# Kernel optimization log

Measured on AMD Instinct MI355X. Metric: run time of the kernel, lower is better.

The kernel has to match this reference:

```python
import jax, jax.numpy as jnp
import numpy as np

HEADS = 8
NEG_SLOPE = 0.2  # PyG GATConv default negative_slope


def segment_softmax(logits, seg, num_segments):
    # logits: [E, H], seg: [E] destination ids
    m = jax.ops.segment_max(logits, seg, num_segments=num_segments)
    m = jnp.where(jnp.isfinite(m), m, 0.0)
    e = jnp.exp(logits - jax.lax.stop_gradient(m)[seg])
    s = jax.ops.segment_sum(e, seg, num_segments=num_segments)
    return e / (s[seg] + 1e-16)


def setup_inputs() -> dict:
    key = jax.random.key(0)
    k1, k2, k3, k4, k5, k6 = jax.random.split(key, 6)
    N, F_IN, H, C, E = 50000, 116, HEADS, 32, 800000
    x = jax.random.normal(k1, (N, F_IN), dtype=jnp.float32)
    edge_index = jax.random.randint(k2, (2, E), 0, N, dtype=jnp.int64)
    # Params (glorot-ish scale)
    W = jax.random.normal(k3, (F_IN, H * C), dtype=jnp.float32) * (1.0 / np.sqrt(F_IN))
    att_src = jax.random.normal(k4, (1, H, C), dtype=jnp.float32) * (1.0 / np.sqrt(C))
    att_dst = jax.random.normal(k5, (1, H, C), dtype=jnp.float32) * (1.0 / np.sqrt(C))
    bias = jnp.zeros((C,), dtype=jnp.float32)
    return {"x": x, "edge_index": edge_index, "W": W, "att_src": att_src, "att_dst": att_dst, "bias": bias}


def reference(x, edge_index, W, att_src, att_dst, bias):
    N = x.shape[0]
    H = HEADS
    C = W.shape[1] // H
    # Shared linear transform: [N, H, C]
    xt = (x @ W).reshape(N, H, C)
    alpha_src = jnp.sum(xt * att_src, axis=-1)  # [N, H]
    alpha_dst = jnp.sum(xt * att_dst, axis=-1)  # [N, H]
    # add_self_loops=True (PyG GATConv default)
    loops = jnp.arange(N, dtype=edge_index.dtype)
    src = jnp.concatenate([edge_index[0], loops])
    dst = jnp.concatenate([edge_index[1], loops])
    # Edge-wise attention logits + segment softmax over destination
    alpha = jax.nn.leaky_relu(alpha_src[src] + alpha_dst[dst], negative_slope=NEG_SLOPE)  # [E', H]
    alpha = segment_softmax(alpha, dst, N)
    # Weighted message aggregation
    msg = xt[src] * alpha[:, :, None]  # [E', H, C]
    out = jax.ops.segment_sum(msg, dst, num_segments=N)  # [N, H, C]
    # concat=False -> mean over heads, then bias
    out = out.mean(axis=1) + bias  # [N, C]
    return jax.nn.relu(out)
```

## Files before the change

kernel.cpp:

```cpp
#include <hip/hip_runtime.h>
#include <hip/hip_bf16.h>


#define F_IN 116
#define HC 256
#define NHEAD 8
#define CDIM 32
#define KP 128
#define ROWS_PB 48
#define DSLOT 64
#define ECHUNK 4096

typedef unsigned int uint32;
typedef short short8 __attribute__((ext_vector_type(8)));
typedef float f32x4 __attribute__((ext_vector_type(4)));

__device__ __forceinline__ unsigned short f2bf(float f) {
    uint32 u = __float_as_uint(f);
    u = (u + 0x7FFF + ((u >> 16) & 1)) >> 16;
    return (unsigned short)u;
}

__global__ void init_k(const float* __restrict__ W,
                       const float* __restrict__ att_s,
                       const float* __restrict__ att_d,
                       unsigned short* __restrict__ WbT,
                       unsigned short* __restrict__ WaT) {
    int idx = blockIdx.x * 256 + threadIdx.x;
    if (idx < 32768) {
        int n = idx >> 7, k = idx & 127;
        WbT[idx] = (k < F_IN) ? f2bf(W[k * HC + n]) : (unsigned short)0;
    } else {
        int aid = idx - 32768;
        int col = aid >> 7, k = aid & 127;
        int tile = col >> 4;
        int cc = col & 15;
        int h = cc & 7, part = cc >> 3;
        const float* att = tile ? att_d : att_s;
        float s = 0.f;
        if (k < F_IN) {
            for (int c = 0; c < CDIM; ++c)
                s = fmaf(W[k * HC + h * CDIM + c], att[h * CDIM + c], s);
        }
        unsigned short hi = f2bf(s);
        unsigned short v = hi;
        if (part) {
            float rem = s - __uint_as_float((uint32)hi << 16);
            v = f2bf(rem);
        }
        WaT[col * KP + k] = v;
    }
}

__global__ __launch_bounds__(256) void scatter_k(const int* __restrict__ src,
                                                 const int* __restrict__ dst,
                                                 int* __restrict__ cnt,
                                                 unsigned short* __restrict__ csr,
                                                 int N, int E) {
    const int t = threadIdx.x;
    const int slice = blockIdx.x & 7;
    const int chunk = blockIdx.x >> 3;
    const int SLICE = (N + 7) >> 3;
    const int lo = slice * SLICE;
    const int hi = (lo + SLICE < N) ? lo + SLICE : N;
    const int ebase = chunk * ECHUNK + t * 4;
#pragma unroll
    for (int it = 0; it < ECHUNK / 1024; ++it) {
        int e = ebase + it * 1024;
        if (e < E) {
            int4 d4 = *(const int4*)&dst[e];
            int4 s4 = *(const int4*)&src[e];
            if (d4.x >= lo && d4.x < hi) {
                int r = atomicAdd(&cnt[d4.x], 1);
                if (r < DSLOT) csr[(d4.x << 6) + r] = (unsigned short)s4.x;
            }
            if (d4.y >= lo && d4.y < hi) {
                int r = atomicAdd(&cnt[d4.y], 1);
                if (r < DSLOT) csr[(d4.y << 6) + r] = (unsigned short)s4.y;
            }
            if (d4.z >= lo && d4.z < hi) {
                int r = atomicAdd(&cnt[d4.z], 1);
                if (r < DSLOT) csr[(d4.z << 6) + r] = (unsigned short)s4.z;
            }
            if (d4.w >= lo && d4.w < hi) {
                int r = atomicAdd(&cnt[d4.w], 1);
                if (r < DSLOT) csr[(d4.w << 6) + r] = (unsigned short)s4.w;
            }
        }
    }
}

__global__ __launch_bounds__(256) void gemm_k(const float* __restrict__ x,
                                              const unsigned short* __restrict__ WbT,
                                              const unsigned short* __restrict__ WaT,
                                              unsigned short* __restrict__ xth,
                                              float* __restrict__ asrc,
                                              float* __restrict__ adst,
                                              int N) {
    const int t = threadIdx.x;
    __shared__ unsigned short xbs[16 * ROWS_PB * 8];
    const int row0 = blockIdx.x * ROWS_PB;
    for (int u = t; u < 16 * ROWS_PB; u += 256) {
        const int g = u / ROWS_PB, r = u - g * ROWS_PB;
        const int gr = row0 + r;
        f32x4 v0 = {0.f, 0.f, 0.f, 0.f}, v1 = {0.f, 0.f, 0.f, 0.f};
        if (gr < N) {
            const f32x4* xp = (const f32x4*)(x + (size_t)gr * F_IN + g * 8);
            if (g < 14) { v0 = xp[0]; v1 = xp[1]; }
            else if (g == 14) { v0 = xp[0]; }
        }
        short8 pk;
        pk[0] = (short)f2bf(v0.x); pk[1] = (short)f2bf(v0.y);
        pk[2] = (short)f2bf(v0.z); pk[3] = (short)f2bf(v0.w);
        pk[4] = (short)f2bf(v1.x); pk[5] = (short)f2bf(v1.y);
        pk[6] = (short)f2bf(v1.z); pk[7] = (short)f2bf(v1.w);
        *(short8*)&xbs[u * 8] = pk;
    }
    __syncthreads();

    const int w = t >> 6, l = t & 63;
    const int q = l >> 4, m = l & 15;
    const int ncol0 = w * 64;

    short8 bfr[4][4];
#pragma unroll
    for (int nt = 0; nt < 4; ++nt)
#pragma unroll
        for (int ks = 0; ks < 4; ++ks)
            bfr[nt][ks] = *(const short8*)&WbT[(size_t)(ncol0 + nt * 16 + m) * KP + ks * 32 + q * 8];

    short8 wa[4];
    if (w < 2) {
#pragma unroll
        for (int ks = 0; ks < 4; ++ks)
            wa[ks] = *(const short8*)&WaT[(size_t)(w * 16 + m) * KP + ks * 32 + q * 8];
    }

    f32x4 acc[3][4];
#pragma unroll
    for (int rt = 0; rt < 3; ++rt)
#pragma unroll
        for (int nt = 0; nt < 4; ++nt) acc[rt][nt] = f32x4{0.f, 0.f, 0.f, 0.f};
    f32x4 acc_a[3];
#pragma unroll
    for (int rt = 0; rt < 3; ++rt) acc_a[rt] = f32x4{0.f, 0.f, 0.f, 0.f};

#pragma unroll
    for (int ks = 0; ks < 4; ++ks) {
        short8 a[3];
#pragma unroll
        for (int rt = 0; rt < 3; ++rt)
            a[rt] = *(const short8*)&xbs[((ks * 4 + q) * ROWS_PB + rt * 16 + m) * 8];
#pragma unroll
        for (int nt = 0; nt < 4; ++nt)
#pragma unroll
            for (int rt = 0; rt < 3; ++rt)
                acc[rt][nt] = __builtin_amdgcn_mfma_f32_16x16x32_bf16(bfr[nt][ks], a[rt], acc[rt][nt], 0, 0, 0);
        if (w < 2) {
#pragma unroll
            for (int rt = 0; rt < 3; ++rt)
                acc_a[rt] = __builtin_amdgcn_mfma_f32_16x16x32_bf16(wa[ks], a[rt], acc_a[rt], 0, 0, 0);
        }
    }

#pragma unroll
    for (int rt = 0; rt < 3; ++rt) {
        const int row = row0 + rt * 16 + m;
        if (row < N) {
#pragma unroll
            for (int nt = 0; nt < 4; ++nt) {
                uint2 pk;
                pk.x = (uint32)f2bf(acc[rt][nt][0]) | ((uint32)f2bf(acc[rt][nt][1]) << 16);
                pk.y = (uint32)f2bf(acc[rt][nt][2]) | ((uint32)f2bf(acc[rt][nt][3]) << 16);
                *(uint2*)&xth[(size_t)row * HC + ncol0 + nt * 16 + q * 4] = pk;
            }
        }
    }

    if (w < 2) {
        float* ap = (w == 0) ? asrc : adst;
#pragma unroll
        for (int rt = 0; rt < 3; ++rt) {
            f32x4 s;
#pragma unroll
            for (int r = 0; r < 4; ++r) {
                float v = acc_a[rt][r];
                s[r] = v + __shfl_xor(v, 32, 64);
            }
            const int row = row0 + rt * 16 + m;
            if (q < 2 && row < N)
                *(f32x4*)&ap[row * NHEAD + q * 4] = s;
        }
    }
}

__global__ __launch_bounds__(256) void aggregate_k(const unsigned short* __restrict__ xth,
                                                   const float* __restrict__ asrc,
                                                   const float* __restrict__ adst,
                                                   const int* __restrict__ cnt,
                                                   const unsigned short* __restrict__ csr,
                                                   const float* __restrict__ bias,
                                                   float* __restrict__ out, int N) {
    const int t = threadIdx.x;
    const int lg = t & 31;
    const int base = t & 32;
    const int n = blockIdx.x * 8 + (t >> 5);
    if (n >= N) return;

    const int h_f = lg >> 2;
    const int h_w = lg & 7;
    const int e_w = lg >> 3;

    const int beg = n << 6;
    int d = cnt[n];
    if (d > DSLOT) d = DSLOT;

    const float adst_hw = adst[n * NHEAD + h_w];

    float zs = asrc[n * NHEAD + h_f] + adst[n * NHEAD + h_f];
    zs = (zs > 0.f) ? zs : 0.2f * zs;
    const float wself = __expf(zs);

    uint4 sv = ((const uint4*)(xth + (size_t)n * HC))[lg];
    float a0 = wself * __uint_as_float(sv.x << 16);
    float a1 = wself * __uint_as_float(sv.x & 0xFFFF0000u);
    float a2 = wself * __uint_as_float(sv.y << 16);
    float a3 = wself * __uint_as_float(sv.y & 0xFFFF0000u);
    float a4 = wself * __uint_as_float(sv.z << 16);
    float a5 = wself * __uint_as_float(sv.z & 0xFFFF0000u);
    float a6 = wself * __uint_as_float(sv.w << 16);
    float a7 = wself * __uint_as_float(sv.w & 0xFFFF0000u);
    float wsum = wself;

    const int nfull = d >> 2;
    const int rem = d & 3;
    int pos = beg;
    for (int cch = 0; cch < nfull; ++cch, pos += 4) {
        int s_w = (int)csr[pos + e_w];
        float z = asrc[s_w * NHEAD + h_w] + adst_hw;
        z = (z > 0.f) ? z : 0.2f * z;
        float w_reg = __expf(z);
#pragma unroll
        for (int e = 0; e < 4; ++e) {
            int s = __shfl(s_w, base + (e << 3), 64);
            float w = __shfl(w_reg, base + (e << 3) + h_f, 64);
            uint4 v = ((const uint4*)(xth + (size_t)s * HC))[lg];
            a0 = fmaf(w, __uint_as_float(v.x << 16), a0);
            a1 = fmaf(w, __uint_as_float(v.x & 0xFFFF0000u), a1);
            a2 = fmaf(w, __uint_as_float(v.y << 16), a2);
            a3 = fmaf(w, __uint_as_float(v.y & 0xFFFF0000u), a3);
            a4 = fmaf(w, __uint_as_float(v.z << 16), a4);
            a5 = fmaf(w, __uint_as_float(v.z & 0xFFFF0000u), a5);
            a6 = fmaf(w, __uint_as_float(v.w << 16), a6);
            a7 = fmaf(w, __uint_as_float(v.w & 0xFFFF0000u), a7);
            wsum += w;
        }
    }
    if (rem) {
        int s_w = (e_w < rem) ? (int)csr[pos + e_w] : n;
        float z = asrc[s_w * NHEAD + h_w] + adst_hw;
        z = (z > 0.f) ? z : 0.2f * z;
        float w_reg = __expf(z);
        for (int e = 0; e < rem; ++e) {
            int s = __shfl(s_w, base + (e << 3), 64);
            float w = __shfl(w_reg, base + (e << 3) + h_f, 64);
            uint4 v = ((const uint4*)(xth + (size_t)s * HC))[lg];
            a0 = fmaf(w, __uint_as_float(v.x << 16), a0);
            a1 = fmaf(w, __uint_as_float(v.x & 0xFFFF0000u), a1);
            a2 = fmaf(w, __uint_as_float(v.y << 16), a2);
            a3 = fmaf(w, __uint_as_float(v.y & 0xFFFF0000u), a3);
            a4 = fmaf(w, __uint_as_float(v.z << 16), a4);
            a5 = fmaf(w, __uint_as_float(v.z & 0xFFFF0000u), a5);
            a6 = fmaf(w, __uint_as_float(v.w << 16), a6);
            a7 = fmaf(w, __uint_as_float(v.w & 0xFFFF0000u), a7);
            wsum += w;
        }
    }

    const float inv = 1.f / (wsum + 1e-16f);
    a0 *= inv; a1 *= inv; a2 *= inv; a3 *= inv;
    a4 *= inv; a5 *= inv; a6 *= inv; a7 *= inv;

#pragma unroll
    for (int o = 4; o <= 16; o <<= 1) {
        a0 += __shfl_xor(a0, o, 64);
        a1 += __shfl_xor(a1, o, 64);
        a2 += __shfl_xor(a2, o, 64);
        a3 += __shfl_xor(a3, o, 64);
        a4 += __shfl_xor(a4, o, 64);
        a5 += __shfl_xor(a5, o, 64);
        a6 += __shfl_xor(a6, o, 64);
        a7 += __shfl_xor(a7, o, 64);
    }

    if (lg < 4) {
        const float* bp = bias + 8 * lg;
        float4 r0, r1;
        r0.x = fmaxf(a0 * 0.125f + bp[0], 0.f);
        r0.y = fmaxf(a1 * 0.125f + bp[1], 0.f);
        r0.z = fmaxf(a2 * 0.125f + bp[2], 0.f);
        r0.w = fmaxf(a3 * 0.125f + bp[3], 0.f);
        r1.x = fmaxf(a4 * 0.125f + bp[4], 0.f);
        r1.y = fmaxf(a5 * 0.125f + bp[5], 0.f);
        r1.z = fmaxf(a6 * 0.125f + bp[6], 0.f);
        r1.w = fmaxf(a7 * 0.125f + bp[7], 0.f);
        *(float4*)&out[(size_t)n * CDIM + 8 * lg] = r0;
        *(float4*)&out[(size_t)n * CDIM + 8 * lg + 4] = r1;
    }
}

extern "C" void kernel_launch(void* const* d_in, const int* in_sizes, int n_in,
                              void* d_out, int out_size, void* d_ws, size_t ws_size,
                              hipStream_t stream) {
    const float* x     = (const float*)d_in[0];
    const int*   ei    = (const int*)d_in[1];
    const float* W     = (const float*)d_in[2];
    const float* att_s = (const float*)d_in[3];
    const float* att_d = (const float*)d_in[4];
    const float* bias  = (const float*)d_in[5];
    float* out = (float*)d_out;

    const int N = in_sizes[0] / F_IN;
    const int E = in_sizes[1] / 2;

    unsigned short* xth = (unsigned short*)d_ws;
    unsigned short* WbT = xth + (size_t)N * HC;
    float* asrc = (float*)(WbT + 256 * KP);
    float* adst = asrc + (size_t)N * NHEAD;
    int*   cnt  = (int*)(adst + (size_t)N * NHEAD);
    unsigned short* csr = (unsigned short*)(cnt + N);
    unsigned short* WaT = csr + (size_t)N * DSLOT;

    const int Ggemm = (N + ROWS_PB - 1) / ROWS_PB;
    const int nchunk = (E + ECHUNK - 1) / ECHUNK;
    const int Gscat = nchunk * 8;

    (void)hipMemsetAsync(cnt, 0, (size_t)N * sizeof(int), stream);
    init_k<<<144, 256, 0, stream>>>(W, att_s, att_d, WbT, WaT);
    scatter_k<<<Gscat, 256, 0, stream>>>(ei, ei + E, cnt, csr, N, E);
    gemm_k<<<Ggemm, 256, 0, stream>>>(x, WbT, WaT, xth, asrc, adst, N);
    aggregate_k<<<(N + 7) / 8, 256, 0, stream>>>(xth, asrc, adst, cnt, csr, bias, out, N);
}
```

Before: 209.9 us.

## Fuse edge scatter and GEMM into one interleaved kernel, fold memset into init

Merges the CSR-building scatter kernel and the feature-transform GEMM kernel into a single launch. Block groups are interleaved in a 3:2 scatter-to-GEMM pattern so the atomic-heavy scatter and the compute-heavy GEMM run at the same time on the GPU. Zeroing of the per-node counters moves from a separate memset into the init kernel. This saves two launches and lets two independent stages overlap, at the cost of a larger fused kernel whose register and LDS footprint applies to scatter blocks too. Any cycles where one side is exhausted leave early-exiting blocks.

```diff
diff --git a/kernel.cpp b/kernel.cpp
--- a/kernel.cpp
+++ b/kernel.cpp
@@ -25,8 +25,10 @@
                        const float* __restrict__ att_s,
                        const float* __restrict__ att_d,
                        unsigned short* __restrict__ WbT,
-                       unsigned short* __restrict__ WaT) {
+                       unsigned short* __restrict__ WaT,
+                       int* __restrict__ cnt, int N) {
     int idx = blockIdx.x * 256 + threadIdx.x;
+    for (int i = idx; i < N; i += 144 * 256) cnt[i] = 0;
     if (idx < 32768) {
         int n = idx >> 7, k = idx & 127;
         WbT[idx] = (k < F_IN) ? f2bf(W[k * HC + n]) : (unsigned short)0;
@@ -52,62 +54,71 @@
     }
 }
 
-__global__ __launch_bounds__(256) void scatter_k(const int* __restrict__ src,
-                                                 const int* __restrict__ dst,
-                                                 int* __restrict__ cnt,
-                                                 unsigned short* __restrict__ csr,
-                                                 int N, int E) {
-    const int t = threadIdx.x;
-    const int slice = blockIdx.x & 7;
-    const int chunk = blockIdx.x >> 3;
-    const int SLICE = (N + 7) >> 3;
-    const int lo = slice * SLICE;
-    const int hi = (lo + SLICE < N) ? lo + SLICE : N;
-    const int ebase = chunk * ECHUNK + t * 4;
-#pragma unroll
-    for (int it = 0; it < ECHUNK / 1024; ++it) {
-        int e = ebase + it * 1024;
-        if (e < E) {
-            int4 d4 = *(const int4*)&dst[e];
-            int4 s4 = *(const int4*)&src[e];
-            if (d4.x >= lo && d4.x < hi) {
-                int r = atomicAdd(&cnt[d4.x], 1);
-                if (r < DSLOT) csr[(d4.x << 6) + r] = (unsigned short)s4.x;
-            }
-            if (d4.y >= lo && d4.y < hi) {
-                int r = atomicAdd(&cnt[d4.y], 1);
-                if (r < DSLOT) csr[(d4.y << 6) + r] = (unsigned short)s4.y;
-            }
-            if (d4.z >= lo && d4.z < hi) {
-                int r = atomicAdd(&cnt[d4.z], 1);
-                if (r < DSLOT) csr[(d4.z << 6) + r] = (unsigned short)s4.z;
-            }
-            if (d4.w >= lo && d4.w < hi) {
-                int r = atomicAdd(&cnt[d4.w], 1);
-                if (r < DSLOT) csr[(d4.w << 6) + r] = (unsigned short)s4.w;
-            }
-        }
-    }
-}
-
-__global__ __launch_bounds__(256) void gemm_k(const float* __restrict__ x,
+__global__ __launch_bounds__(256) void fuse_k(const float* __restrict__ x,
                                               const unsigned short* __restrict__ WbT,
                                               const unsigned short* __restrict__ WaT,
                                               unsigned short* __restrict__ xth,
                                               float* __restrict__ asrc,
                                               float* __restrict__ adst,
-                                              int N) {
+                                              int N, int nScatGrp, int Ggemm,
+                                              const int* __restrict__ src,
+                                              const int* __restrict__ dst,
+                                              int* __restrict__ cnt,
+                                              unsigned short* __restrict__ csr, int E) {
     const int t = threadIdx.x;
+    const int g = blockIdx.x >> 3, r = blockIdx.x & 7;
+    const int c = g / 5, p = g - c * 5;
+
+    if (p < 3) {
+        const int sg = c * 3 + p;
+        if (sg >= nScatGrp) return;
+        const int sbid = sg * 8 + r;
+        const int slice = sbid & 7;
+        const int chunk = sbid >> 3;
+        const int SLICE = (N + 7) >> 3;
+        const int lo = slice * SLICE;
+        const int hi = (lo + SLICE < N) ? lo + SLICE : N;
+        const int ebase = chunk * ECHUNK + t * 4;
+#pragma unroll
+        for (int it = 0; it < ECHUNK / 1024; ++it) {
+            int e = ebase + it * 1024;
+            if (e < E) {
+                int4 d4 = *(const int4*)&dst[e];
+                int4 s4 = *(const int4*)&src[e];
+                if (d4.x >= lo && d4.x < hi) {
+                    int rr = atomicAdd(&cnt[d4.x], 1);
+                    if (rr < DSLOT) csr[(d4.x << 6) + rr] = (unsigned short)s4.x;
+                }
+                if (d4.y >= lo && d4.y < hi) {
+                    int rr = atomicAdd(&cnt[d4.y], 1);
+                    if (rr < DSLOT) csr[(d4.y << 6) + rr] = (unsigned short)s4.y;
+                }
+                if (d4.z >= lo && d4.z < hi) {
+                    int rr = atomicAdd(&cnt[d4.z], 1);
+                    if (rr < DSLOT) csr[(d4.z << 6) + rr] = (unsigned short)s4.z;
+                }
+                if (d4.w >= lo && d4.w < hi) {
+                    int rr = atomicAdd(&cnt[d4.w], 1);
+                    if (rr < DSLOT) csr[(d4.w << 6) + rr] = (unsigned short)s4.w;
+                }
+            }
+        }
+        return;
+    }
+
+    const int gbid = (c * 2 + (p - 3)) * 8 + r;
+    if (gbid >= Ggemm) return;
+
     __shared__ unsigned short xbs[16 * ROWS_PB * 8];
-    const int row0 = blockIdx.x * ROWS_PB;
+    const int row0 = gbid * ROWS_PB;
     for (int u = t; u < 16 * ROWS_PB; u += 256) {
-        const int g = u / ROWS_PB, r = u - g * ROWS_PB;
-        const int gr = row0 + r;
+        const int gg = u / ROWS_PB, rr = u - gg * ROWS_PB;
+        const int gr = row0 + rr;
         f32x4 v0 = {0.f, 0.f, 0.f, 0.f}, v1 = {0.f, 0.f, 0.f, 0.f};
         if (gr < N) {
-            const f32x4* xp = (const f32x4*)(x + (size_t)gr * F_IN + g * 8);
-            if (g < 14) { v0 = xp[0]; v1 = xp[1]; }
-            else if (g == 14) { v0 = xp[0]; }
+            const f32x4* xp = (const f32x4*)(x + (size_t)gr * F_IN + gg * 8);
+            if (gg < 14) { v0 = xp[0]; v1 = xp[1]; }
+            else if (gg == 14) { v0 = xp[0]; }
         }
         short8 pk;
         pk[0] = (short)f2bf(v0.x); pk[1] = (short)f2bf(v0.y);
@@ -183,9 +194,9 @@
         for (int rt = 0; rt < 3; ++rt) {
             f32x4 s;
 #pragma unroll
-            for (int r = 0; r < 4; ++r) {
-                float v = acc_a[rt][r];
-                s[r] = v + __shfl_xor(v, 32, 64);
+            for (int rr = 0; rr < 4; ++rr) {
+                float v = acc_a[rt][rr];
+                s[rr] = v + __shfl_xor(v, 32, 64);
             }
             const int row = row0 + rt * 16 + m;
             if (q < 2 && row < N)
@@ -334,10 +345,16 @@
     const int Ggemm = (N + ROWS_PB - 1) / ROWS_PB;
     const int nchunk = (E + ECHUNK - 1) / ECHUNK;
     const int Gscat = nchunk * 8;
-
-    (void)hipMemsetAsync(cnt, 0, (size_t)N * sizeof(int), stream);
-    init_k<<<144, 256, 0, stream>>>(W, att_s, att_d, WbT, WaT);
-    scatter_k<<<Gscat, 256, 0, stream>>>(ei, ei + E, cnt, csr, N, E);
-    gemm_k<<<Ggemm, 256, 0, stream>>>(x, WbT, WaT, xth, asrc, adst, N);
+    const int nScatGrp = (Gscat + 7) / 8;
+    const int nGemmGrp = (Ggemm + 7) / 8;
+    const int cS = (nScatGrp + 2) / 3;
+    const int cG = (nGemmGrp + 1) / 2;
+    const int ncyc = (cS > cG) ? cS : cG;
+    const int Gfuse = ncyc * 5 * 8;
+
+    init_k<<<144, 256, 0, stream>>>(W, att_s, att_d, WbT, WaT, cnt, N);
+    fuse_k<<<Gfuse, 256, 0, stream>>>(x, WbT, WaT, xth, asrc, adst,
+                                      N, nScatGrp, Ggemm,
+                                      ei, ei + E, cnt, csr, E);
     aggregate_k<<<(N + 7) / 8, 256, 0, stream>>>(xth, asrc, adst, cnt, csr, bias, out, N);
 }
```

After: 201.3 us. -4.1%, faster.
